# Kernel optimization log

Measured on AMD Instinct MI355X. Metric: run time of the kernel, lower is better.

The kernel has to match this reference:

```python
import jax, jax.numpy as jnp
import numpy as np

N_NODES = 100000
N_EDGES = 1600000
F_IN = 64
F_HID = 64
CURV = 1.0          # fixed curvature for every layer (args.c)
MIN_NORM = 1e-15    # HGCN min_norm clamp
PROJ_EPS = 4e-3     # HGCN float32 boundary eps


def _artanh(x):
    x = jnp.clip(x, -1.0 + 1e-7, 1.0 - 1e-7)
    return 0.5 * (jnp.log1p(x) - jnp.log1p(-x))


def _norm(x):
    return jnp.sqrt(jnp.clip(jnp.sum(x * x, axis=-1, keepdims=True), MIN_NORM))


def proj(x, c):
    # clip points to the open Poincare ball of radius (1-eps)/sqrt(c)
    maxnorm = (1.0 - PROJ_EPS) / jnp.sqrt(c)
    n = _norm(x)
    return jnp.where(n > maxnorm, x / n * maxnorm, x)


def expmap0(u, c):
    sc = jnp.sqrt(c)
    n = _norm(u)
    return jnp.tanh(sc * n) * u / (sc * n)


def logmap0(p, c):
    sc = jnp.sqrt(c)
    n = _norm(p)
    return _artanh(sc * n) * p / (sc * n)


def mobius_add(x, y, c):
    x2 = jnp.sum(x * x, -1, keepdims=True)
    y2 = jnp.sum(y * y, -1, keepdims=True)
    xy = jnp.sum(x * y, -1, keepdims=True)
    num = (1.0 + 2.0 * c * xy + c * y2) * x + (1.0 - c * x2) * y
    den = 1.0 + 2.0 * c * xy + c * c * x2 * y2
    return num / jnp.clip(den, MIN_NORM)


def mobius_matvec(M, x, c):
    sc = jnp.sqrt(c)
    xn = _norm(x)
    mx = x @ M.T                       # [N, out]
    mxn = _norm(mx)
    res = jnp.tanh(mxn / xn * _artanh(sc * xn)) * mx / (mxn * sc)
    zero = jnp.all(mx == 0, axis=-1, keepdims=True)
    return jnp.where(zero, jnp.zeros_like(res), res)


def hyp_linear(x, W, b, c):
    res = proj(mobius_matvec(W, x, c), c)
    hyp_b = proj(expmap0(b.reshape(1, -1), c), c)   # proj_tan0 is identity on Poincare ball
    return proj(mobius_add(res, hyp_b, c), c)


def hyp_agg(x, src, dst, w, c, n_nodes):
    xt = logmap0(x, c)                              # tangent space at origin
    msg = xt[src] * w[:, None]                      # [E, d] gather + weight
    agg = jax.ops.segment_sum(msg, dst, num_segments=n_nodes)  # spmm(adj, xt)
    return proj(expmap0(agg, c), c)


def hyp_act(x, c_in, c_out):
    xt = jax.nn.relu(logmap0(x, c_in))              # act in tangent space
    return proj(expmap0(xt, c_out), c_out)          # proj_tan0 identity


def hgnn_layer(x, W, b, src, dst, w, c_in, c_out, n_nodes):
    h = hyp_linear(x, W, b, c_in)
    h = hyp_agg(h, src, dst, w, c_in, n_nodes)
    return hyp_act(h, c_in, c_out)


def setup_inputs() -> dict:
    key = jax.random.key(0)
    ks = jax.random.split(key, 7)
    x = jax.random.normal(ks[0], (N_NODES, F_IN), dtype=jnp.float32)
    edge_index = jax.random.randint(ks[1], (2, N_EDGES), 0, N_NODES, dtype=jnp.int64 if jax.config.jax_enable_x64 else jnp.int32)
    edge_weight = jax.random.uniform(ks[2], (N_EDGES,), dtype=jnp.float32) / 16.0
    W0 = jax.random.normal(ks[3], (F_HID, F_IN), dtype=jnp.float32) * 0.1
    b0 = jax.random.normal(ks[4], (F_HID,), dtype=jnp.float32) * 0.1
    W1 = jax.random.normal(ks[5], (F_HID, F_HID), dtype=jnp.float32) * 0.1
    b1 = jax.random.normal(ks[6], (F_HID,), dtype=jnp.float32) * 0.1
    return {"x": x, "edge_index": edge_index, "edge_weight": edge_weight,
            "W0": W0, "b0": b0, "W1": W1, "b1": b1}


def reference(x, edge_index, edge_weight, W0, b0, W1, b1):
    src, dst = edge_index[0], edge_index[1]
    # encode(): proj_tan0 (identity for Poincare ball) -> expmap0 -> proj
    h = proj(expmap0(x, CURV), CURV)
    h = hgnn_layer(h, W0, b0, src, dst, edge_weight, CURV, CURV, N_NODES)
    h = hgnn_layer(h, W1, b1, src, dst, edge_weight, CURV, CURV, N_NODES)
    return h
```

## Files before the change

### kernel.cpp

```cpp
#include <hip/hip_runtime.h>
#include <hip/hip_bf16.h>
#include <stdint.h>

#define MIN_NORM 1e-15f
#define MAXNORM 0.996f
#define ART_CLIP 0.9999999f
#define CAP 5120
#define BKT_NODES 256
#define W_SCALE 524288.f
#define W_INV   (1.f / 524288.f)
#define CUR_STRIDE 16

typedef __attribute__((ext_vector_type(8))) short s8v;
typedef __attribute__((ext_vector_type(4))) float f4v;

__device__ __forceinline__ float rcp_f(float x) { return __builtin_amdgcn_rcpf(x); }

__device__ __forceinline__ float fast_tanh(float x) {
    float e = __expf(2.f * x);
    return 1.f - 2.f * rcp_f(e + 1.f);
}
__device__ __forceinline__ float fast_artanh(float x) {
    x = fminf(x, ART_CLIP);
    return 0.5f * __logf((1.f + x) * rcp_f(1.f - x));
}

__device__ __forceinline__ float wsum(float v) {
#pragma unroll
    for (int m = 32; m >= 1; m >>= 1) v += __shfl_xor(v, m, 64);
    return v;
}
__device__ __forceinline__ unsigned wave_iscan(unsigned v, int lane) {
#pragma unroll
    for (int d = 1; d < 64; d <<= 1) {
        unsigned o = __shfl_up(v, d, 64);
        if (lane >= d) v += o;
    }
    return v;
}

__device__ __forceinline__ unsigned short f2bf(float f) {
    unsigned u = __builtin_bit_cast(unsigned, f);
    u += 0x7FFFu + ((u >> 16) & 1u);
    return (unsigned short)(u >> 16);
}
__device__ __forceinline__ float bf2f(unsigned short h) {
    return __builtin_bit_cast(float, (unsigned)h << 16);
}
__device__ __forceinline__ float bfu_lo(unsigned v) {
    return __builtin_bit_cast(float, v << 16);
}
__device__ __forceinline__ float bfu_hi(unsigned v) {
    return __builtin_bit_cast(float, v & 0xFFFF0000u);
}

__device__ __forceinline__ void part_body(const int* __restrict__ dst,
                                          const int* __restrict__ src,
                                          const float* __restrict__ ew,
                                          unsigned* __restrict__ bktCur,
                                          int2* __restrict__ part, int E, int NB,
                                          int blk, int PB) {
    __shared__ unsigned lcnt[512], lbase[512];
    const int tid = threadIdx.x;
    const int chunk = (E + PB - 1) / PB;
    const int lo = blk * chunk, hi = min(lo + chunk, E);
    for (int i = tid; i < NB; i += 256) lcnt[i] = 0;
    __syncthreads();
    for (int e = lo + tid; e < hi; e += 256)
        atomicAdd(&lcnt[(unsigned)dst[e] >> 8], 1u);
    __syncthreads();
    for (int i = tid; i < NB; i += 256) {
        unsigned c = lcnt[i];
        lbase[i] = c ? atomicAdd(&bktCur[i * CUR_STRIDE], c) : 0u;
        lcnt[i] = 0;
    }
    __syncthreads();
    for (int e = lo + tid; e < hi; e += 256) {
        int d = dst[e];
        int bkt = (unsigned)d >> 8;
        unsigned r = atomicAdd(&lcnt[bkt], 1u);
        unsigned rel = lbase[bkt] + r;
        if (rel < CAP)
            part[(size_t)bkt * CAP + rel] =
                make_int2(((d & 255) << 17) | src[e], __float_as_int(ew[e]));
    }
}

__global__ void __launch_bounds__(256) k_sort(const int2* __restrict__ part,
                                              const unsigned* __restrict__ bktCur,
                                              unsigned* __restrict__ part2,
                                              int2* __restrict__ off2, int nNodes) {
    const int b = blockIdx.x;
    const int base = b * CAP;
    const int cnt = min((int)bktCur[b * CUR_STRIDE], CAP);
    const int tid = threadIdx.x, lane = tid & 63, wid = tid >> 6;
    __shared__ unsigned hist[256];
    __shared__ unsigned wpart[4];
    hist[tid] = 0;
    __syncthreads();
    for (int i = tid; i < cnt; i += 256)
        atomicAdd(&hist[(unsigned)part[base + i].x >> 17], 1u);
    __syncthreads();
    unsigned h = hist[tid];
    unsigned inc = wave_iscan(h, lane);
    if (lane == 63) wpart[wid] = inc;
    __syncthreads();
    unsigned wo = 0;
    for (int i = 0; i < wid; ++i) wo += wpart[i];
    unsigned start = wo + inc - h;
    int node = b * BKT_NODES + tid;
    if (node < nNodes)
        off2[node] = make_int2(base + (int)start, base + (int)(start + h));
    __syncthreads();
    hist[tid] = start;
    __syncthreads();
    for (int i = tid; i < cnt; i += 256) {
        int2 m = part[base + i];
        unsigned r = atomicAdd(&hist[(unsigned)m.x >> 17], 1u);
        float w = __int_as_float(m.y);
        unsigned fw = (unsigned)__float2uint_rn(w * W_SCALE);
        if (fw > 32767u) fw = 32767u;
        part2[base + r] = (fw << 17) | ((unsigned)m.x & 0x1FFFFu);
    }
}

template <bool ENCODE>
__device__ __forceinline__ void lin_scalars(float n2, float m2, float d, float y2,
                                            float& lam, float& mu) {
    float nx = sqrtf(fmaxf(n2, MIN_NORM));
    float xn = ENCODE ? fminf(fast_tanh(nx), MAXNORM) : nx;
    float sm = sqrtf(fmaxf(m2, MIN_NORM));
    float ratio = sm * rcp_f(nx);
    float tt = fminf(fast_tanh(ratio * fast_artanh(xn)), MAXNORM);
    float rho = tt * rcp_f(sm);
    float xy = rho * d;
    float x2 = tt * tt;
    float den = fmaxf(1.f + 2.f * xy + x2 * y2, MIN_NORM);
    float iden = rcp_f(den);
    float A = (1.f + 2.f * xy + y2) * iden;
    float B = (1.f - x2) * iden;
    float on2 = A * A * x2 + 2.f * A * B * xy + B * B * y2;
    float on = sqrtf(fmaxf(on2, MIN_NORM));
    float g = on > MAXNORM ? MAXNORM * rcp_f(on) : 1.f;
    float onc = fminf(on, MAXNORM);
    float L = fast_artanh(onc) * rcp_f(onc) * g;
    lam = L * A * rho;
    mu  = L * B;
}

template <bool ENCODE>
__device__ __forceinline__ void lin_body(const float* __restrict__ xin,
                                         const float* __restrict__ W,
                                         const float* __restrict__ braw,
                                         unsigned short* __restrict__ xt_out,
                                         int nNodes, int nTiles, int blk, int LB) {
    __shared__ float shb[65];
    const int tid = threadIdx.x;
    if (tid < 64) {
        float u = braw[tid];
        float n = sqrtf(fmaxf(wsum(u * u), MIN_NORM));
        float t = tanhf(n);
        float h = t * u / n;
        float hn = sqrtf(fmaxf(wsum(h * h), MIN_NORM));
        if (hn > MAXNORM) h *= MAXNORM / hn;
        shb[tid] = h;
        float y2 = wsum(h * h);
        if (tid == 0) shb[64] = y2;
    }
    __syncthreads();

    const int lane = tid & 63, wid = tid >> 6;
    const int col = lane & 15, q = lane >> 4;

    s8v wfh[4][2], wfl[4][2];
    float hbr[4][4];
#pragma unroll
    for (int f = 0; f < 4; ++f) {
#pragma unroll
        for (int s = 0; s < 2; ++s) {
            const float4 a4 = *(const float4*)(W + (size_t)(16 * f + col) * 64 + 4 * q + 32 * s);
            const float4 b4 = *(const float4*)(W + (size_t)(16 * f + col) * 64 + 4 * q + 16 + 32 * s);
            float v[8] = {a4.x, a4.y, a4.z, a4.w, b4.x, b4.y, b4.z, b4.w};
            s8v h8, l8;
#pragma unroll
            for (int e = 0; e < 8; ++e) {
                unsigned short hb_ = f2bf(v[e]);
                float hf = bf2f(hb_);
                h8[e] = (short)hb_;
                l8[e] = (short)f2bf(v[e] - hf);
            }
            wfh[f][s] = h8;
            wfl[f][s] = l8;
        }
#pragma unroll
        for (int r = 0; r < 4; ++r) hbr[f][r] = shb[16 * f + 4 * q + r];
    }
    const float y2 = shb[64];

    const int nw = LB * 4;
    for (int t = blk * 4 + wid; t < nTiles; t += nw) {
        const int node = t * 16 + col;
        const bool ok = node < nNodes;
        const int ldn = ok ? node : (nNodes - 1);
        float n2p = 0.f;
        s8v xh[2], xl[2];
#pragma unroll
        for (int s = 0; s < 2; ++s) {
            const float4 a4 = *(const float4*)(xin + (size_t)ldn * 64 + 4 * q + 32 * s);
            const float4 b4 = *(const float4*)(xin + (size_t)ldn * 64 + 4 * q + 16 + 32 * s);
            float xv[8] = {a4.x, a4.y, a4.z, a4.w, b4.x, b4.y, b4.z, b4.w};
            s8v h8, l8;
#pragma unroll
            for (int e = 0; e < 8; ++e) {
                float xe = xv[e];
                n2p = fmaf(xe, xe, n2p);
                unsigned short hb_ = f2bf(xe);
                float hf = bf2f(hb_);
                h8[e] = (short)hb_;
                l8[e] = (short)f2bf(xe - hf);
            }
            xh[s] = h8;
            xl[s] = l8;
        }
        f4v acc[4];
#pragma unroll
        for (int f = 0; f < 4; ++f) acc[f] = (f4v){0.f, 0.f, 0.f, 0.f};
#pragma unroll
        for (int s = 0; s < 2; ++s) {
#pragma unroll
            for (int f = 0; f < 4; ++f)
                acc[f] = __builtin_amdgcn_mfma_f32_16x16x32_bf16(wfh[f][s], xh[s], acc[f], 0, 0, 0);
#pragma unroll
            for (int f = 0; f < 4; ++f)
                acc[f] = __builtin_amdgcn_mfma_f32_16x16x32_bf16(wfh[f][s], xl[s], acc[f], 0, 0, 0);
#pragma unroll
            for (int f = 0; f < 4; ++f)
                acc[f] = __builtin_amdgcn_mfma_f32_16x16x32_bf16(wfl[f][s], xh[s], acc[f], 0, 0, 0);
        }
        float m2p = 0.f, dp = 0.f;
#pragma unroll
        for (int f = 0; f < 4; ++f)
#pragma unroll
            for (int r = 0; r < 4; ++r) {
                float mv = acc[f][r];
                m2p = fmaf(mv, mv, m2p);
                dp  = fmaf(mv, hbr[f][r], dp);
            }
#pragma unroll
        for (int m = 16; m <= 32; m <<= 1) {
            n2p += __shfl_xor(n2p, m, 64);
            m2p += __shfl_xor(m2p, m, 64);
            dp  += __shfl_xor(dp,  m, 64);
        }
        float lam, mu;
        lin_scalars<ENCODE>(n2p, m2p, dp, y2, lam, mu);
        if (ok) {
#pragma unroll
            for (int f = 0; f < 4; ++f) {
                float r0 = fmaf(lam, acc[f][0], mu * hbr[f][0]);
                float r1 = fmaf(lam, acc[f][1], mu * hbr[f][1]);
                float r2 = fmaf(lam, acc[f][2], mu * hbr[f][2]);
                float r3 = fmaf(lam, acc[f][3], mu * hbr[f][3]);
                uint2 pk;
                pk.x = (unsigned)f2bf(r0) | ((unsigned)f2bf(r1) << 16);
                pk.y = (unsigned)f2bf(r2) | ((unsigned)f2bf(r3) << 16);
                *(uint2*)(xt_out + (size_t)node * 64 + 16 * f + 4 * q) = pk;
            }
        }
    }
}

__global__ void __launch_bounds__(256, 2) k_pre(const int* __restrict__ dst,
                                                const int* __restrict__ src,
                                                const float* __restrict__ ew,
                                                unsigned* __restrict__ bktCur,
                                                int2* __restrict__ part, int E, int NB,
                                                const float* __restrict__ x,
                                                const float* __restrict__ W0,
                                                const float* __restrict__ b0,
                                                unsigned short* __restrict__ xt,
                                                int nNodes, int nTiles, int PB, int LB) {
    if ((int)blockIdx.x < PB)
        part_body(dst, src, ew, bktCur, part, E, NB, blockIdx.x, PB);
    else
        lin_body<true>(x, W0, b0, xt, nNodes, nTiles, blockIdx.x - PB, LB);
}

template <bool ENCODE>
__global__ void __launch_bounds__(256, 2) k_lin(const float* __restrict__ xin,
                                                const float* __restrict__ W,
                                                const float* __restrict__ braw,
                                                unsigned short* __restrict__ xt_out,
                                                int nNodes, int nTiles) {
    lin_body<ENCODE>(xin, W, braw, xt_out, nNodes, nTiles, blockIdx.x, gridDim.x);
}

__global__ void __launch_bounds__(256) k_agg(const unsigned short* __restrict__ xt,
                                             const unsigned* __restrict__ meta,
                                             const int2* __restrict__ off2,
                                             float* __restrict__ hout, int nNodes) {
    const int tid = threadIdx.x;
    const int lane = tid & 63;
    const int h = lane >> 5;
    const int j = lane & 31;
    const int hbase = h << 5;
    const int nw = gridDim.x * (blockDim.x >> 6);
    const int nPairs = (nNodes + 1) >> 1;
    int pair = blockIdx.x * (blockDim.x >> 6) + (tid >> 6);
    if (pair >= nPairs) return;
    int node = pair * 2 + h;
    int2 rng = (node < nNodes) ? off2[node] : make_int2(0, 0);
    while (true) {
        const int nxt = pair + nw;
        int2 rngN = make_int2(0, 0);
        if (nxt < nPairs) {
            int nn = nxt * 2 + h;
            if (nn < nNodes) rngN = off2[nn];
        }
        const bool okn = node < nNodes;
        const int s0 = rng.x;
        const int deg = rng.y - rng.x;
        unsigned mp = 0;
        if (j < deg) mp = meta[s0 + j];
        const int kmax = min(deg, 32);
        const int kOther = __shfl(kmax, lane ^ 32, 64);
        const int kCeil = (max(kmax, kOther) + 7) & ~7;
        float a0 = 0.f, a1 = 0.f, b0_ = 0.f, b1_ = 0.f;
        for (int k = 0; k < kCeil; k += 8) {
            unsigned p0 = __shfl(mp, hbase + k, 64);
            unsigned p1 = __shfl(mp, hbase + k + 1, 64);
            unsigned p2 = __shfl(mp, hbase + k + 2, 64);
            unsigned p3 = __shfl(mp, hbase + k + 3, 64);
            unsigned p4 = __shfl(mp, hbase + k + 4, 64);
            unsigned p5 = __shfl(mp, hbase + k + 5, 64);
            unsigned p6 = __shfl(mp, hbase + k + 6, 64);
            unsigned p7 = __shfl(mp, hbase + k + 7, 64);
            unsigned v0 = *(const unsigned*)(xt + (((p0 & 0x1FFFFu) << 6) + 2 * j));
            unsigned v1 = *(const unsigned*)(xt + (((p1 & 0x1FFFFu) << 6) + 2 * j));
            unsigned v2 = *(const unsigned*)(xt + (((p2 & 0x1FFFFu) << 6) + 2 * j));
            unsigned v3 = *(const unsigned*)(xt + (((p3 & 0x1FFFFu) << 6) + 2 * j));
            unsigned v4 = *(const unsigned*)(xt + (((p4 & 0x1FFFFu) << 6) + 2 * j));
            unsigned v5 = *(const unsigned*)(xt + (((p5 & 0x1FFFFu) << 6) + 2 * j));
            unsigned v6 = *(const unsigned*)(xt + (((p6 & 0x1FFFFu) << 6) + 2 * j));
            unsigned v7 = *(const unsigned*)(xt + (((p7 & 0x1FFFFu) << 6) + 2 * j));
            float w0 = (float)(p0 >> 17);
            float w1 = (float)(p1 >> 17);
            float w2 = (float)(p2 >> 17);
            float w3 = (float)(p3 >> 17);
            float w4 = (float)(p4 >> 17);
            float w5 = (float)(p5 >> 17);
            float w6 = (float)(p6 >> 17);
            float w7 = (float)(p7 >> 17);
            a0 = fmaf(bfu_lo(v0), w0, a0);   a1 = fmaf(bfu_hi(v0), w0, a1);
            b0_ = fmaf(bfu_lo(v1), w1, b0_); b1_ = fmaf(bfu_hi(v1), w1, b1_);
            a0 = fmaf(bfu_lo(v2), w2, a0);   a1 = fmaf(bfu_hi(v2), w2, a1);
            b0_ = fmaf(bfu_lo(v3), w3, b0_); b1_ = fmaf(bfu_hi(v3), w3, b1_);
            a0 = fmaf(bfu_lo(v4), w4, a0);   a1 = fmaf(bfu_hi(v4), w4, a1);
            b0_ = fmaf(bfu_lo(v5), w5, b0_); b1_ = fmaf(bfu_hi(v5), w5, b1_);
            a0 = fmaf(bfu_lo(v6), w6, a0);   a1 = fmaf(bfu_hi(v6), w6, a1);
            b0_ = fmaf(bfu_lo(v7), w7, b0_); b1_ = fmaf(bfu_hi(v7), w7, b1_);
        }
        for (int kk = s0 + 32; kk < rng.y; ++kk) {
            unsigned pv = meta[kk];
            unsigned v = *(const unsigned*)(xt + (((pv & 0x1FFFFu) << 6) + 2 * j));
            float wv2 = (float)(pv >> 17);
            a0 = fmaf(bfu_lo(v), wv2, a0);
            a1 = fmaf(bfu_hi(v), wv2, a1);
        }
        float acc0 = (a0 + b0_) * W_INV, acc1 = (a1 + b1_) * W_INV;
        float r0 = fmaxf(acc0, 0.f), r1 = fmaxf(acc1, 0.f);
        float sA = fmaf(acc0, acc0, acc1 * acc1);
        float sR = fmaf(r0, r0, r1 * r1);
#pragma unroll
        for (int mm = 1; mm <= 16; mm <<= 1) {
            sA += __shfl_xor(sA, mm, 64);
            sR += __shfl_xor(sR, mm, 64);
        }
        float n = sqrtf(fmaxf(sA, MIN_NORM));
        float t = fast_tanh(n);
        float g1 = t > MAXNORM ? MAXNORM * rcp_f(t) : 1.f;
        float tc = fminf(t, MAXNORM);
        float alpha = fast_artanh(tc) * rcp_f(tc) * g1 * t * rcp_f(n);
        float mnorm = sqrtf(fmaxf(alpha * alpha * sR, MIN_NORM));
        float t2 = fast_tanh(mnorm);
        float g2 = t2 > MAXNORM ? MAXNORM * rcp_f(t2) : 1.f;
        float gamma = t2 * rcp_f(mnorm) * g2 * alpha;
        if (okn) {
            float2 o;
            o.x = gamma * r0;
            o.y = gamma * r1;
            *(float2*)(hout + (size_t)node * 64 + 2 * j) = o;
        }
        if (nxt >= nPairs) break;
        pair = nxt;
        node = pair * 2 + h;
        rng = rngN;
    }
}

extern "C" void kernel_launch(void* const* d_in, const int* in_sizes, int n_in,
                              void* d_out, int out_size, void* d_ws, size_t ws_size,
                              hipStream_t stream) {
    const float* x   = (const float*)d_in[0];
    const int*   ei  = (const int*)d_in[1];
    const float* ew  = (const float*)d_in[2];
    const float* W0  = (const float*)d_in[3];
    const float* b0  = (const float*)d_in[4];
    const float* W1  = (const float*)d_in[5];
    const float* b1  = (const float*)d_in[6];
    const int N = in_sizes[0] / 64;
    const int E = in_sizes[2];
    const int* src = ei;
    const int* dst = ei + E;
    const int NB = (N + BKT_NODES - 1) / BKT_NODES;
    const int nTiles = (N + 15) / 16;
    const int PB = 256, LB = 1024;

    uint8_t* p = (uint8_t*)d_ws;
    auto carve = [&](size_t bytes) { uint8_t* q = p; p += (bytes + 255) & ~(size_t)255; return q; };
    unsigned*       bktCur = (unsigned*)carve((size_t)NB * CUR_STRIDE * 4);
    int2*           part   = (int2*)carve((size_t)NB * CAP * 8);
    unsigned*       part2  = (unsigned*)carve((size_t)NB * CAP * 4);
    int2*           off2   = (int2*)carve((size_t)N * 8);
    unsigned short* xt     = (unsigned short*)carve((size_t)N * 64 * 2);
    float*          hbuf   = (float*)d_out;

    hipMemsetAsync(bktCur, 0, (size_t)NB * CUR_STRIDE * 4, stream);
    k_pre<<<PB + LB, 256, 0, stream>>>(dst, src, ew, bktCur, part, E, NB,
                                       x, W0, b0, xt, N, nTiles, PB, LB);
    k_sort<<<NB, 256, 0, stream>>>(part, bktCur, part2, off2, N);

    k_agg<<<2048, 256, 0, stream>>>(xt, part2, off2, hbuf, N);
    k_lin<false><<<1024, 256, 0, stream>>>(hbuf, W1, b1, xt, N, nTiles);
    k_agg<<<2048, 256, 0, stream>>>(xt, part2, off2, (float*)d_out, N);
}
```

Measured before the change: 154.6 us.

## Split fused partition/linear kernel into separate launches; widen partition blocks and agg grid

Breaks up the combined k_pre kernel, which ran edge partitioning and the encode linear layer side by side, into a separate k_part kernel launched with 1024-thread blocks and a standalone k_lin<true> launch. The aggregation kernels now launch with 4096 blocks instead of 2048. The aim is to give each phase a launch configuration suited to its own work, at the cost of losing the overlap between partitioning and the linear layer and adding one extra kernel launch.

After: 151.7 us. About the same (-1.9%).

```diff
diff --git a/kernel.cpp b/kernel.cpp
--- a/kernel.cpp
+++ b/kernel.cpp
@@ -54,28 +54,29 @@
     return __builtin_bit_cast(float, v & 0xFFFF0000u);
 }
 
-__device__ __forceinline__ void part_body(const int* __restrict__ dst,
-                                          const int* __restrict__ src,
-                                          const float* __restrict__ ew,
-                                          unsigned* __restrict__ bktCur,
-                                          int2* __restrict__ part, int E, int NB,
-                                          int blk, int PB) {
+__global__ void __launch_bounds__(1024) k_part(const int* __restrict__ dst,
+                                               const int* __restrict__ src,
+                                               const float* __restrict__ ew,
+                                               unsigned* __restrict__ bktCur,
+                                               int2* __restrict__ part, int E, int NB) {
     __shared__ unsigned lcnt[512], lbase[512];
     const int tid = threadIdx.x;
+    const int BT = blockDim.x;
+    const int PB = gridDim.x;
     const int chunk = (E + PB - 1) / PB;
-    const int lo = blk * chunk, hi = min(lo + chunk, E);
-    for (int i = tid; i < NB; i += 256) lcnt[i] = 0;
-    __syncthreads();
-    for (int e = lo + tid; e < hi; e += 256)
+    const int lo = blockIdx.x * chunk, hi = min(lo + chunk, E);
+    for (int i = tid; i < NB; i += BT) lcnt[i] = 0;
+    __syncthreads();
+    for (int e = lo + tid; e < hi; e += BT)
         atomicAdd(&lcnt[(unsigned)dst[e] >> 8], 1u);
     __syncthreads();
-    for (int i = tid; i < NB; i += 256) {
+    for (int i = tid; i < NB; i += BT) {
         unsigned c = lcnt[i];
         lbase[i] = c ? atomicAdd(&bktCur[i * CUR_STRIDE], c) : 0u;
         lcnt[i] = 0;
     }
     __syncthreads();
-    for (int e = lo + tid; e < hi; e += 256) {
+    for (int e = lo + tid; e < hi; e += BT) {
         int d = dst[e];
         int bkt = (unsigned)d >> 8;
         unsigned r = atomicAdd(&lcnt[bkt], 1u);
@@ -149,11 +150,11 @@
 }
 
 template <bool ENCODE>
-__device__ __forceinline__ void lin_body(const float* __restrict__ xin,
-                                         const float* __restrict__ W,
-                                         const float* __restrict__ braw,
-                                         unsigned short* __restrict__ xt_out,
-                                         int nNodes, int nTiles, int blk, int LB) {
+__global__ void __launch_bounds__(256, 2) k_lin(const float* __restrict__ xin,
+                                                const float* __restrict__ W,
+                                                const float* __restrict__ braw,
+                                                unsigned short* __restrict__ xt_out,
+                                                int nNodes, int nTiles) {
     __shared__ float shb[65];
     const int tid = threadIdx.x;
     if (tid < 64) {
@@ -197,8 +198,8 @@
     }
     const float y2 = shb[64];
 
-    const int nw = LB * 4;
-    for (int t = blk * 4 + wid; t < nTiles; t += nw) {
+    const int nw = gridDim.x * 4;
+    for (int t = blockIdx.x * 4 + wid; t < nTiles; t += nw) {
         const int node = t * 16 + col;
         const bool ok = node < nNodes;
         const int ldn = ok ? node : (nNodes - 1);
@@ -268,31 +269,6 @@
             }
         }
     }
-}
-
-__global__ void __launch_bounds__(256, 2) k_pre(const int* __restrict__ dst,
-                                                const int* __restrict__ src,
-                                                const float* __restrict__ ew,
-                                                unsigned* __restrict__ bktCur,
-                                                int2* __restrict__ part, int E, int NB,
-                                                const float* __restrict__ x,
-                                                const float* __restrict__ W0,
-                                                const float* __restrict__ b0,
-                                                unsigned short* __restrict__ xt,
-                                                int nNodes, int nTiles, int PB, int LB) {
-    if ((int)blockIdx.x < PB)
-        part_body(dst, src, ew, bktCur, part, E, NB, blockIdx.x, PB);
-    else
-        lin_body<true>(x, W0, b0, xt, nNodes, nTiles, blockIdx.x - PB, LB);
-}
-
-template <bool ENCODE>
-__global__ void __launch_bounds__(256, 2) k_lin(const float* __restrict__ xin,
-                                                const float* __restrict__ W,
-                                                const float* __restrict__ braw,
-                                                unsigned short* __restrict__ xt_out,
-                                                int nNodes, int nTiles) {
-    lin_body<ENCODE>(xin, W, braw, xt_out, nNodes, nTiles, blockIdx.x, gridDim.x);
 }
 
 __global__ void __launch_bounds__(256) k_agg(const unsigned short* __restrict__ xt,
@@ -414,7 +390,6 @@
     const int* dst = ei + E;
     const int NB = (N + BKT_NODES - 1) / BKT_NODES;
     const int nTiles = (N + 15) / 16;
-    const int PB = 256, LB = 1024;
 
     uint8_t* p = (uint8_t*)d_ws;
     auto carve = [&](size_t bytes) { uint8_t* q = p; p += (bytes + 255) & ~(size_t)255; return q; };
@@ -426,11 +401,10 @@
     float*          hbuf   = (float*)d_out;
 
     hipMemsetAsync(bktCur, 0, (size_t)NB * CUR_STRIDE * 4, stream);
-    k_pre<<<PB + LB, 256, 0, stream>>>(dst, src, ew, bktCur, part, E, NB,
-                                       x, W0, b0, xt, N, nTiles, PB, LB);
+    k_part<<<256, 1024, 0, stream>>>(dst, src, ew, bktCur, part, E, NB);
     k_sort<<<NB, 256, 0, stream>>>(part, bktCur, part2, off2, N);
-
-    k_agg<<<2048, 256, 0, stream>>>(xt, part2, off2, hbuf, N);
+    k_lin<true><<<1024, 256, 0, stream>>>(x, W0, b0, xt, N, nTiles);
+    k_agg<<<4096, 256, 0, stream>>>(xt, part2, off2, hbuf, N);
     k_lin<false><<<1024, 256, 0, stream>>>(hbuf, W1, b1, xt, N, nTiles);
-    k_agg<<<2048, 256, 0, stream>>>(xt, part2, off2, (float*)d_out, N);
-}
+    k_agg<<<4096, 256, 0, stream>>>(xt, part2, off2, (float*)d_out, N);
+}
```
